# Performance work log

Hardware: AMD Instinct MI355X
Metric: run time of the kernel (lower is better)

The kernel has to match this reference:

```python
import jax, jax.numpy as jnp
import numpy as np

K = 3  # kernel_size
KK = K * K


def conv2d(x, w, b, stride=1, padding=1, dilation=1):
    out = jax.lax.conv_general_dilated(
        x, w, (stride, stride), [(padding, padding), (padding, padding)],
        rhs_dilation=(dilation, dilation),
        dimension_numbers=('NCHW', 'OIHW', 'NCHW'))
    return out + b[None, :, None, None]


def bilinear_gather(x, py, px):
    # x: [B,C,H,W]; py,px: [B,KK,H,W] float sampling coords (zero outside).
    B, C, H, W = x.shape
    y0 = jnp.floor(py)
    x0 = jnp.floor(px)
    wy1 = py - y0
    wx1 = px - x0
    xf = x.reshape(B, C, H * W)

    def corner(yc, xc, wgt):
        valid = (yc >= 0) & (yc <= H - 1) & (xc >= 0) & (xc <= W - 1)
        yi = jnp.clip(yc, 0, H - 1).astype(jnp.int32)
        xi = jnp.clip(xc, 0, W - 1).astype(jnp.int32)
        idx = (yi * W + xi).reshape(B, 1, -1)  # [B,1,KK*H*W]
        v = jnp.take_along_axis(xf, jnp.broadcast_to(idx, (B, C, idx.shape[-1])), axis=2)
        v = v.reshape(B, C, *yc.shape[1:])  # [B,C,KK,H,W]
        return v * (wgt * valid)[:, None]

    return (corner(y0, x0, (1 - wy1) * (1 - wx1)) +
            corner(y0, x0 + 1, (1 - wy1) * wx1) +
            corner(y0 + 1, x0, wy1 * (1 - wx1)) +
            corner(y0 + 1, x0 + 1, wy1 * wx1))


def modulated_deform_conv(x, offset, mask, w, b, stride=1, padding=1, dilation=1):
    B, C, H, W = x.shape
    Ho, Wo = offset.shape[2], offset.shape[3]
    off = offset.reshape(B, KK, 2, Ho, Wo)
    dy, dx = off[:, :, 0], off[:, :, 1]  # [B,KK,Ho,Wo]
    ki, kj = jnp.meshgrid(jnp.arange(K), jnp.arange(K), indexing='ij')
    ki = ki.reshape(-1).astype(x.dtype)  # [KK]
    kj = kj.reshape(-1).astype(x.dtype)
    base_y = (jnp.arange(Ho) * stride - padding).astype(x.dtype)
    base_x = (jnp.arange(Wo) * stride - padding).astype(x.dtype)
    py = base_y[None, None, :, None] + (ki * dilation)[None, :, None, None] + dy
    px = base_x[None, None, None, :] + (kj * dilation)[None, :, None, None] + dx
    x_off = bilinear_gather(x, py, px)              # [B,C,KK,Ho,Wo]
    x_off = x_off * mask[:, None]                   # modulation
    w_flat = w.reshape(w.shape[0], C, KK)           # [O,C,KK]
    out = jnp.einsum('bckhw,ock->bohw', x_off, w_flat)
    return out + b[None, :, None, None]


def setup_inputs() -> dict:
    key = jax.random.key(0)
    ks = jax.random.split(key, 7)
    B, C, O, H, W = 8, 64, 64, 128, 128
    x = jax.random.normal(ks[0], (B, C, H, W), dtype=jnp.float32)
    # offset/mask predictor convs (zero-init in the module; randomized small here
    # so offsets/masks are non-trivial for kernel correctness testing)
    p_w = jax.random.normal(ks[1], (2 * KK, C, 3, 3), dtype=jnp.float32) * 0.02
    p_b = jax.random.normal(ks[2], (2 * KK,), dtype=jnp.float32) * 0.1
    m_w = jax.random.normal(ks[3], (KK, C, 3, 3), dtype=jnp.float32) * 0.02
    m_b = jax.random.normal(ks[4], (KK,), dtype=jnp.float32) * 0.1
    # deformable conv weights
    d_w = jax.random.normal(ks[5], (O, C, K, K), dtype=jnp.float32) * (1.0 / np.sqrt(C * KK))
    d_b = jax.random.normal(ks[6], (O,), dtype=jnp.float32) * 0.01
    return {"x": x, "p_w": p_w, "p_b": p_b, "m_w": m_w, "m_b": m_b, "d_w": d_w, "d_b": d_b}


def reference(x, p_w, p_b, m_w, m_b, d_w, d_b):
    offset = conv2d(x, p_w, p_b, stride=1, padding=1, dilation=1)   # [B,18,H,W]
    mask = jax.nn.sigmoid(conv2d(x, m_w, m_b, stride=1, padding=1, dilation=1))  # [B,9,H,W]
    out = modulated_deform_conv(x, offset, mask, d_w, d_b, stride=1, padding=1, dilation=1)
    return (out, offset)
```

## Files before the change

kernel.cpp:

```cpp
#include <hip/hip_runtime.h>
#include <math.h>

#define KK 9
#define BB 8
#define CC 64
#define OO 64
#define HH 128
#define WW 128
#define HWSZ (HH*WW)

typedef _Float16 half8 __attribute__((ext_vector_type(8)));
typedef float    floatx4 __attribute__((ext_vector_type(4)));

#define WP_ELEMS (32*576)
#define WD_ELEMS (9*64*64)
#define XH_ELEMS ((size_t)BB*HWSZ*64)
#define NCONV 2048

__global__ __launch_bounds__(256) void prep(
    const float* __restrict__ x,
    const float* __restrict__ p_w, const float* __restrict__ m_w,
    const float* __restrict__ d_w,
    _Float16* __restrict__ Wp, _Float16* __restrict__ Wd, _Float16* __restrict__ x_h,
    int conv_blocks)
{
    const int blk = blockIdx.x;
    const int tid = threadIdx.x;
    if (blk < conv_blocks) {
        __shared__ _Float16 sh[64][72];
        const int b    = blk >> 8;
        const int pix0 = (blk & 255) * 64;
        const float* xb = x + (size_t)b*CC*HWSZ + pix0;
        {
            const int p     = tid & 63;
            const int cbase = tid >> 6;
            #pragma unroll
            for (int j = 0; j < 16; ++j) {
                const int c = j*4 + cbase;
                sh[p][c] = (_Float16)xb[(size_t)c*HWSZ + p];
            }
        }
        __syncthreads();
        {
            const int p  = tid >> 2;
            const int c0 = (tid & 3) * 16;
            _Float16* dst = x_h + ((size_t)b*HWSZ + pix0 + p)*64 + c0;
            *(half8*)dst       = *(const half8*)&sh[p][c0];
            *(half8*)(dst + 8) = *(const half8*)&sh[p][c0 + 8];
        }
    } else {
        const int i = (blk - conv_blocks)*256 + tid;
        if (i < WP_ELEMS) {
            int n = i / 576, r = i % 576;
            int k = r >> 6, c = r & 63;
            float v = 0.f;
            if (n < 18)      v = p_w[(n*CC + c)*KK + k];
            else if (n < 27) v = m_w[((n-18)*CC + c)*KK + k];
            Wp[i] = (_Float16)v;
        } else if (i < WP_ELEMS + WD_ELEMS) {
            int j = i - WP_ELEMS;
            int k = j / 4096, r = j % 4096, o = r >> 6, c = r & 63;
            Wd[j] = (_Float16)d_w[(o*CC + c)*KK + k];
        }
    }
}

__global__ __launch_bounds__(512, 4) void dcn_fused(
    const _Float16* __restrict__ x_h,
    const _Float16* __restrict__ Wp, const _Float16* __restrict__ Wd,
    const float* __restrict__ p_b, const float* __restrict__ m_b,
    const float* __restrict__ db,
    float* __restrict__ out, float* __restrict__ offset_out)
{
    __shared__ alignas(16) char smem[128*72*2 + 64*72*2];
    _Float16* AS = (_Float16*)smem;
    _Float16* WS = (_Float16*)(smem + 128*72*2);

    const int tid  = threadIdx.x;
    const int wv   = tid >> 6;
    const int lane = tid & 63;
    const int quad = lane >> 4;
    const int l15  = lane & 15;
    const int p    = tid & 127;
    const int cq   = tid >> 7;
    const int b    = blockIdx.x & 7;
    const int row  = blockIdx.x >> 3;
    const int pix0 = row * WW;
    const _Float16* xbh = x_h + (size_t)b*HWSZ*64;

    half8 q0, q1, pw1;
    bool vldc = false;
    auto issue1 = [&](int k) {
        const int hy = row + k/3 - 1;
        const int wx = p   + k%3 - 1;
        vldc = (hy >= 0) & (hy < HH) & (wx >= 0) & (wx < WW);
        const _Float16* ap = xbh + (size_t)(vldc ? hy*WW + wx : 0)*64 + cq*16;
        q0 = *(const half8*)ap;
        q1 = *(const half8*)(ap + 8);
        if (tid < 256)
            pw1 = *(const half8*)(Wp + (tid>>3)*576 + k*64 + (tid&7)*8);
    };

    floatx4 accp[2];
    accp[0] = (floatx4)0.f; accp[1] = (floatx4)0.f;

    issue1(0);
    #pragma unroll
    for (int k = 0; k < 9; ++k) {
        if (tid < 256)
            *(half8*)&WS[(tid>>3)*72 + (tid&7)*8] = pw1;
        const half8 z = (half8)(_Float16)0.f;
        *(half8*)&AS[p*72 + cq*16]     = vldc ? q0 : z;
        *(half8*)&AS[p*72 + cq*16 + 8] = vldc ? q1 : z;
        __syncthreads();
        if (k < 8) issue1(k+1);
        #pragma unroll
        for (int ks = 0; ks < 2; ++ks) {
            half8 bf0 = *(const half8*)&WS[(l15     )*72 + ks*32 + quad*8];
            half8 bf1 = *(const half8*)&WS[(16 + l15)*72 + ks*32 + quad*8];
            half8 af  = *(const half8*)&AS[(wv*16 + l15)*72 + ks*32 + quad*8];
            accp[0] = __builtin_amdgcn_mfma_f32_16x16x32_f16(af, bf0, accp[0], 0, 0, 0);
            accp[1] = __builtin_amdgcn_mfma_f32_16x16x32_f16(af, bf1, accp[1], 0, 0, 0);
        }
        __syncthreads();
    }

    float* T = (float*)AS;
    #pragma unroll
    for (int nt = 0; nt < 2; ++nt) {
        const int ch = nt*16 + l15;
        if (ch < 27) {
            #pragma unroll
            for (int r = 0; r < 4; ++r)
                T[ch*132 + wv*16 + quad*4 + r] = accp[nt][r];
        }
    }
    __syncthreads();

    float dyk[9], dxk[9], mkk[9];
    #pragma unroll
    for (int k = 0; k < 9; ++k) {
        dyk[k] = T[(2*k  )*132 + p] + p_b[2*k];
        dxk[k] = T[(2*k+1)*132 + p] + p_b[2*k+1];
        mkk[k] = 1.f / (1.f + expf(-(T[(18+k)*132 + p] + m_b[k])));
    }
    {
        float* offp = offset_out + (size_t)b*18*HWSZ + pix0;
        #pragma unroll
        for (int j = 0; j < 5; ++j) {
            const int idx = j*512 + tid;
            if (idx < 2304) {
                const int ch = idx >> 7, px = idx & 127;
                offp[ch*HWSZ + px] = T[ch*132 + px] + p_b[ch];
            }
        }
    }
    __syncthreads();

    half8 pa[8], pwv;
    float phw[4];
    auto issue2 = [&](int k) {
        const float py = (float)(row - 1 + k/3) + dyk[k];
        const float px = (float)(p   - 1 + k%3) + dxk[k];
        const float mk = mkk[k];
        const float y0f = floorf(py), x0f = floorf(px);
        const int   iy0 = (int)y0f,   ix0 = (int)x0f;
        const float wy1 = py - y0f,   wx1 = px - x0f;
        const float wy0 = 1.f - wy1,  wx0 = 1.f - wx1;
        const bool vy0 = (iy0   >= 0) & (iy0   < HH);
        const bool vy1 = (iy0+1 >= 0) & (iy0+1 < HH);
        const bool vx0 = (ix0   >= 0) & (ix0   < WW);
        const bool vx1 = (ix0+1 >= 0) & (ix0+1 < WW);
        const int cy0 = min(max(iy0,   0), HH-1), cy1 = min(max(iy0+1, 0), HH-1);
        const int cx0 = min(max(ix0,   0), WW-1), cx1 = min(max(ix0+1, 0), WW-1);
        const int i0 = cy0*WW+cx0, i1 = cy0*WW+cx1, i2 = cy1*WW+cx0, i3 = cy1*WW+cx1;
        phw[0] = wy0*wx0*((vy0&vx0) ? mk : 0.f);
        phw[1] = wy0*wx1*((vy0&vx1) ? mk : 0.f);
        phw[2] = wy1*wx0*((vy1&vx0) ? mk : 0.f);
        phw[3] = wy1*wx1*((vy1&vx1) ? mk : 0.f);
        const _Float16* c0p = xbh + (size_t)i0*64 + cq*16;
        const _Float16* c1p = xbh + (size_t)i1*64 + cq*16;
        const _Float16* c2p = xbh + (size_t)i2*64 + cq*16;
        const _Float16* c3p = xbh + (size_t)i3*64 + cq*16;
        pa[0] = *(const half8*)c0p;  pa[1] = *(const half8*)(c0p + 8);
        pa[2] = *(const half8*)c1p;  pa[3] = *(const half8*)(c1p + 8);
        pa[4] = *(const half8*)c2p;  pa[5] = *(const half8*)(c2p + 8);
        pa[6] = *(const half8*)c3p;  pa[7] = *(const half8*)(c3p + 8);
        pwv = *(const half8*)(Wd + k*4096 + tid*8);
    };

    floatx4 acc[4];
    #pragma unroll
    for (int nt = 0; nt < 4; ++nt) acc[nt] = (floatx4)0.f;

    issue2(0);
    #pragma unroll
    for (int k = 0; k < 9; ++k) {
        *(half8*)&WS[(tid>>3)*72 + (tid&7)*8] = pwv;
        const _Float16 g0 = (_Float16)phw[0], g1 = (_Float16)phw[1],
                       g2 = (_Float16)phw[2], g3 = (_Float16)phw[3];
        half8 lo = pa[0]*g0 + pa[2]*g1 + pa[4]*g2 + pa[6]*g3;
        half8 hi = pa[1]*g0 + pa[3]*g1 + pa[5]*g2 + pa[7]*g3;
        *(half8*)&AS[p*72 + cq*16]     = lo;
        *(half8*)&AS[p*72 + cq*16 + 8] = hi;
        __syncthreads();
        if (k < 8) issue2(k+1);
        #pragma unroll
        for (int ks = 0; ks < 2; ++ks) {
            half8 af = *(const half8*)&AS[(wv*16 + l15)*72 + ks*32 + quad*8];
            #pragma unroll
            for (int nt = 0; nt < 4; ++nt) {
                half8 bf = *(const half8*)&WS[(nt*16 + l15)*72 + ks*32 + quad*8];
                acc[nt] = __builtin_amdgcn_mfma_f32_16x16x32_f16(af, bf, acc[nt], 0, 0, 0);
            }
        }
        __syncthreads();
    }

    float* T2 = (float*)AS;
    #pragma unroll
    for (int oc = 0; oc < 4; ++oc) {
        #pragma unroll
        for (int r = 0; r < 4; ++r)
            T2[l15*132 + wv*16 + quad*4 + r] = acc[oc][r];
        __syncthreads();
        #pragma unroll
        for (int j = 0; j < 4; ++j) {
            const int idx = j*512 + tid;
            const int o16 = idx >> 7, p2 = idx & 127;
            out[((size_t)b*OO + oc*16 + o16)*HWSZ + pix0 + p2] = T2[o16*132 + p2] + db[oc*16 + o16];
        }
        __syncthreads();
    }
}

__global__ __launch_bounds__(256, 4) void dcn_fused_lds(
    const float* __restrict__ x,
    const _Float16* __restrict__ Wp, const _Float16* __restrict__ Wd,
    const float* __restrict__ p_b, const float* __restrict__ m_b,
    const float* __restrict__ db,
    float* __restrict__ out, float* __restrict__ offset_out)
{
    __shared__ alignas(16) _Float16 A_sh[128][72];
    __shared__ alignas(16) _Float16 WM_sh[32*72];
    __shared__ alignas(16) _Float16 Wd_sh[64][72];

    const int tid   = threadIdx.x;
    const int wv    = tid >> 6;
    const int lane  = tid & 63;
    const int quad  = lane >> 4;
    const int l15   = lane & 15;
    const int b     = blockIdx.x & 7;
    const int row   = blockIdx.x >> 3;
    const int pix0  = row * WW;
    const int p     = tid & 127;
    const int chalf = (tid >> 7) * 32;
    const int h = row, w = p;
    const float* xb = x + (size_t)b*CC*HWSZ;
    _Float16 (*W_sh)[72] = (_Float16 (*)[72])WM_sh;

    floatx4 accp[2][2];
    #pragma unroll
    for (int mt = 0; mt < 2; ++mt)
        #pragma unroll
        for (int nt = 0; nt < 2; ++nt) accp[mt][nt] = (floatx4)0.f;

    for (int k = 0; k < 9; ++k) {
        {
            const int n  = tid >> 3;
            const int c0 = (tid & 7) * 8;
            *(half8*)&W_sh[n][c0] = *(const half8*)(Wp + n*576 + k*64 + c0);
        }
        const int hy = h + (k/3) - 1;
        const int wx = w + (k%3) - 1;
        const bool vld = (hy >= 0) & (hy < HH) & (wx >= 0) & (wx < WW);
        const float* xs = xb + hy*WW + wx;
        #pragma unroll
        for (int cb = 0; cb < 4; ++cb) {
            union { half8 v; _Float16 e[8]; } u;
            #pragma unroll
            for (int j = 0; j < 8; ++j)
                u.e[j] = (_Float16)(vld ? xs[(size_t)(chalf + cb*8 + j)*HWSZ] : 0.f);
            *(half8*)&A_sh[p][chalf + cb*8] = u.v;
        }
        __syncthreads();
        #pragma unroll
        for (int ks = 0; ks < 2; ++ks) {
            half8 bf[2];
            #pragma unroll
            for (int nt = 0; nt < 2; ++nt)
                bf[nt] = *(const half8*)&W_sh[nt*16 + l15][ks*32 + quad*8];
            #pragma unroll
            for (int mt = 0; mt < 2; ++mt) {
                half8 af = *(const half8*)&A_sh[wv*32 + mt*16 + l15][ks*32 + quad*8];
                accp[mt][0] = __builtin_amdgcn_mfma_f32_16x16x32_f16(af, bf[0], accp[mt][0], 0, 0, 0);
                accp[mt][1] = __builtin_amdgcn_mfma_f32_16x16x32_f16(af, bf[1], accp[mt][1], 0, 0, 0);
            }
        }
        __syncthreads();
    }

    float (*T)[132] = (float (*)[132])&A_sh[0][0];
    #pragma unroll
    for (int nt = 0; nt < 2; ++nt) {
        const int ch = nt*16 + l15;
        if (ch < 27) {
            #pragma unroll
            for (int mt = 0; mt < 2; ++mt)
                #pragma unroll
                for (int r = 0; r < 4; ++r)
                    T[ch][wv*32 + mt*16 + quad*4 + r] = accp[mt][nt][r];
        }
    }
    __syncthreads();

    float dyk[9], dxk[9], mkk[9];
    float* offp = offset_out + (size_t)b*18*HWSZ + pix0;
    #pragma unroll
    for (int k = 0; k < 9; ++k) {
        dyk[k] = T[2*k][p]   + p_b[2*k];
        dxk[k] = T[2*k+1][p] + p_b[2*k+1];
        mkk[k] = 1.f / (1.f + expf(-(T[18+k][p] + m_b[k])));
    }
    if (tid < 128) {
        #pragma unroll
        for (int k = 0; k < 9; ++k) {
            offp[(2*k  )*HWSZ + p] = dyk[k];
            offp[(2*k+1)*HWSZ + p] = dxk[k];
        }
    }
    __syncthreads();

    floatx4 acc[2][4];
    #pragma unroll
    for (int mt = 0; mt < 2; ++mt)
        #pragma unroll
        for (int nt = 0; nt < 4; ++nt) acc[mt][nt] = (floatx4)0.f;

    for (int k = 0; k < 9; ++k) {
        {
            const int o  = tid >> 2;
            const int c0 = (tid & 3) * 16;
            const _Float16* src = Wd + k*4096 + o*64 + c0;
            *(half8*)&Wd_sh[o][c0]     = *(const half8*)src;
            *(half8*)&Wd_sh[o][c0 + 8] = *(const half8*)(src + 8);
        }
        const float mk = mkk[k];
        const float py = (float)(h - 1 + k/3) + dyk[k];
        const float px = (float)(w - 1 + k%3) + dxk[k];
        const float y0f = floorf(py), x0f = floorf(px);
        const int   iy0 = (int)y0f,   ix0 = (int)x0f;
        const float wy1 = py - y0f,   wx1 = px - x0f;
        const float wy0 = 1.f - wy1,  wx0 = 1.f - wx1;
        const bool vy0 = (iy0   >= 0) & (iy0   < HH);
        const bool vy1 = (iy0+1 >= 0) & (iy0+1 < HH);
        const bool vx0 = (ix0   >= 0) & (ix0   < WW);
        const bool vx1 = (ix0+1 >= 0) & (ix0+1 < WW);
        const int cy0 = min(max(iy0,   0), HH-1), cy1 = min(max(iy0+1, 0), HH-1);
        const int cx0 = min(max(ix0,   0), WW-1), cx1 = min(max(ix0+1, 0), WW-1);
        const int i0 = cy0*WW+cx0; const float w0 = wy0*wx0*((vy0&vx0) ? mk : 0.f);
        const int i1 = cy0*WW+cx1; const float w1 = wy0*wx1*((vy0&vx1) ? mk : 0.f);
        const int i2 = cy1*WW+cx0; const float w2 = wy1*wx0*((vy1&vx0) ? mk : 0.f);
        const int i3 = cy1*WW+cx1; const float w3 = wy1*wx1*((vy1&vx1) ? mk : 0.f);
        #pragma unroll
        for (int cb = 0; cb < 4; ++cb) {
            union { half8 v; _Float16 e[8]; } u;
            #pragma unroll
            for (int j = 0; j < 8; ++j) {
                const float* xc = xb + (size_t)(chalf + cb*8 + j)*HWSZ;
                u.e[j] = (_Float16)(w0*xc[i0] + w1*xc[i1] + w2*xc[i2] + w3*xc[i3]);
            }
            *(half8*)&A_sh[p][chalf + cb*8] = u.v;
        }
        __syncthreads();
        #pragma unroll
        for (int ks = 0; ks < 2; ++ks) {
            half8 bf[4];
            #pragma unroll
            for (int nt = 0; nt < 4; ++nt)
                bf[nt] = *(const half8*)&Wd_sh[nt*16 + l15][ks*32 + quad*8];
            #pragma unroll
            for (int mt = 0; mt < 2; ++mt) {
                half8 af = *(const half8*)&A_sh[wv*32 + mt*16 + l15][ks*32 + quad*8];
                #pragma unroll
                for (int nt = 0; nt < 4; ++nt)
                    acc[mt][nt] = __builtin_amdgcn_mfma_f32_16x16x32_f16(af, bf[nt], acc[mt][nt], 0, 0, 0);
            }
        }
        __syncthreads();
    }

    float (*T2)[132] = (float (*)[132])&A_sh[0][0];
    #pragma unroll
    for (int oc = 0; oc < 4; ++oc) {
        #pragma unroll
        for (int mt = 0; mt < 2; ++mt)
            #pragma unroll
            for (int r = 0; r < 4; ++r)
                T2[l15][wv*32 + mt*16 + quad*4 + r] = acc[mt][oc][r];
        __syncthreads();
        #pragma unroll
        for (int j = 0; j < 8; ++j) {
            const int idx = tid + j*256;
            const int o16 = idx >> 7, p2 = idx & 127;
            out[((size_t)b*OO + oc*16 + o16)*HWSZ + pix0 + p2] = T2[o16][p2] + db[oc*16 + o16];
        }
        __syncthreads();
    }
}

extern "C" void kernel_launch(void* const* d_in, const int* in_sizes, int n_in,
                              void* d_out, int out_size, void* d_ws, size_t ws_size,
                              hipStream_t stream) {
    const float* x   = (const float*)d_in[0];
    const float* p_w = (const float*)d_in[1];
    const float* p_b = (const float*)d_in[2];
    const float* m_w = (const float*)d_in[3];
    const float* m_b = (const float*)d_in[4];
    const float* dw  = (const float*)d_in[5];
    const float* db  = (const float*)d_in[6];

    float* out        = (float*)d_out;
    float* offset_out = out + (size_t)BB*OO*HWSZ;

    _Float16* Wp  = (_Float16*)d_ws;
    _Float16* Wd  = Wp + WP_ELEMS;
    _Float16* x_h = Wd + WD_ELEMS;

    const int nrep = (WP_ELEMS + WD_ELEMS + 255) / 256;
    const size_t need = (size_t)(WP_ELEMS + WD_ELEMS + XH_ELEMS) * sizeof(_Float16);
    if (ws_size >= need) {
        prep<<<dim3(NCONV + nrep), 256, 0, stream>>>(x, p_w, m_w, dw, Wp, Wd, x_h, NCONV);
        dcn_fused<<<dim3(128*BB), 512, 0, stream>>>(x_h, Wp, Wd, p_b, m_b, db, out, offset_out);
    } else {
        prep<<<dim3(nrep), 256, 0, stream>>>(x, p_w, m_w, dw, Wp, Wd, x_h, 0);
        dcn_fused_lds<<<dim3(128*BB), 256, 0, stream>>>(x, Wp, Wd, p_b, m_b, db, out, offset_out);
    }
}
```

Before: 184.1 us.

## Pre-swizzle weights into MFMA fragment order and load operands directly from global

The prep kernel now writes the predictor and deform weights in the per-lane MFMA fragment layout, so the fused kernel reads A and B operands straight from global memory instead of staging them through LDS. The fused kernel is retiled to half-row blocks of 64 pixels with 256 threads, twice as many blocks, and only the deform weights are double-buffered in LDS with one barrier per tap. Offset and mask values are read from a shared table per tap instead of held in registers, and the bias is folded in once. This removes most LDS traffic and barriers, in exchange for more redundant global gathers of x_h per pixel tile and more blocks that each reload the weights.

Measured after the change: 187.9 us. +2.1%, slower.

```diff
diff --git a/kernel.cpp b/kernel.cpp
--- a/kernel.cpp
+++ b/kernel.cpp
@@ -12,8 +12,8 @@
 typedef _Float16 half8 __attribute__((ext_vector_type(8)));
 typedef float    floatx4 __attribute__((ext_vector_type(4)));
 
-#define WP_ELEMS (32*576)
-#define WD_ELEMS (9*64*64)
+#define WP_ELEMS (9*2*4*32*8)
+#define WD_ELEMS (9*2*4*64*8)
 #define XH_ELEMS ((size_t)BB*HWSZ*64)
 #define NCONV 2048
 
@@ -51,184 +51,173 @@
     } else {
         const int i = (blk - conv_blocks)*256 + tid;
         if (i < WP_ELEMS) {
-            int n = i / 576, r = i % 576;
-            int k = r >> 6, c = r & 63;
+            const int e = i & 7, n = (i>>3)&31, quad = (i>>8)&3, ks = (i>>10)&1, k = i>>11;
+            const int c = ks*32 + quad*8 + e;
             float v = 0.f;
             if (n < 18)      v = p_w[(n*CC + c)*KK + k];
             else if (n < 27) v = m_w[((n-18)*CC + c)*KK + k];
             Wp[i] = (_Float16)v;
         } else if (i < WP_ELEMS + WD_ELEMS) {
-            int j = i - WP_ELEMS;
-            int k = j / 4096, r = j % 4096, o = r >> 6, c = r & 63;
+            const int j = i - WP_ELEMS;
+            const int e = j & 7, o = (j>>3)&63, quad = (j>>9)&3, ks = (j>>11)&1, k = j>>12;
+            const int c = ks*32 + quad*8 + e;
             Wd[j] = (_Float16)d_w[(o*CC + c)*KK + k];
         }
     }
 }
 
-__global__ __launch_bounds__(512, 4) void dcn_fused(
+__global__ __launch_bounds__(256, 4) void dcn_fused(
     const _Float16* __restrict__ x_h,
     const _Float16* __restrict__ Wp, const _Float16* __restrict__ Wd,
     const float* __restrict__ p_b, const float* __restrict__ m_b,
     const float* __restrict__ db,
     float* __restrict__ out, float* __restrict__ offset_out)
 {
-    __shared__ alignas(16) char smem[128*72*2 + 64*72*2];
-    _Float16* AS = (_Float16*)smem;
-    _Float16* WS = (_Float16*)(smem + 128*72*2);
+    __shared__ alignas(16) float    T[27*68];
+    __shared__ alignas(16) _Float16 WS[2][4096];
 
     const int tid  = threadIdx.x;
     const int wv   = tid >> 6;
     const int lane = tid & 63;
     const int quad = lane >> 4;
     const int l15  = lane & 15;
-    const int p    = tid & 127;
-    const int cq   = tid >> 7;
     const int b    = blockIdx.x & 7;
-    const int row  = blockIdx.x >> 3;
-    const int pix0 = row * WW;
+    const int seg  = blockIdx.x >> 3;
+    const int row  = seg >> 1;
+    const int col0 = (seg & 1) * 64;
+    const int pix0 = row * WW + col0;
+    const int px   = wv*16 + l15;
+    const int wx   = col0 + px;
     const _Float16* xbh = x_h + (size_t)b*HWSZ*64;
 
-    half8 q0, q1, pw1;
-    bool vldc = false;
-    auto issue1 = [&](int k) {
-        const int hy = row + k/3 - 1;
-        const int wx = p   + k%3 - 1;
-        vldc = (hy >= 0) & (hy < HH) & (wx >= 0) & (wx < WW);
-        const _Float16* ap = xbh + (size_t)(vldc ? hy*WW + wx : 0)*64 + cq*16;
-        q0 = *(const half8*)ap;
-        q1 = *(const half8*)(ap + 8);
-        if (tid < 256)
-            pw1 = *(const half8*)(Wp + (tid>>3)*576 + k*64 + (tid&7)*8);
-    };
+    half8 ws0a = *(const half8*)(Wd + tid*16);
+    half8 ws0b = *(const half8*)(Wd + tid*16 + 8);
 
     floatx4 accp[2];
     accp[0] = (floatx4)0.f; accp[1] = (floatx4)0.f;
-
-    issue1(0);
     #pragma unroll
     for (int k = 0; k < 9; ++k) {
-        if (tid < 256)
-            *(half8*)&WS[(tid>>3)*72 + (tid&7)*8] = pw1;
+        const int hy = row + k/3 - 1;
+        const int hx = wx  + k%3 - 1;
+        const bool vld = (hy >= 0) & (hy < HH) & (hx >= 0) & (hx < WW);
+        const _Float16* ap = xbh + (size_t)(vld ? hy*WW + hx : 0)*64 + quad*8;
         const half8 z = (half8)(_Float16)0.f;
-        *(half8*)&AS[p*72 + cq*16]     = vldc ? q0 : z;
-        *(half8*)&AS[p*72 + cq*16 + 8] = vldc ? q1 : z;
-        __syncthreads();
-        if (k < 8) issue1(k+1);
+        half8 a0 = *(const half8*)ap;
+        half8 a1 = *(const half8*)(ap + 32);
+        a0 = vld ? a0 : z;
+        a1 = vld ? a1 : z;
+        const _Float16* wp = Wp + k*2048 + quad*256 + l15*8;
         #pragma unroll
         for (int ks = 0; ks < 2; ++ks) {
-            half8 bf0 = *(const half8*)&WS[(l15     )*72 + ks*32 + quad*8];
-            half8 bf1 = *(const half8*)&WS[(16 + l15)*72 + ks*32 + quad*8];
-            half8 af  = *(const half8*)&AS[(wv*16 + l15)*72 + ks*32 + quad*8];
-            accp[0] = __builtin_amdgcn_mfma_f32_16x16x32_f16(af, bf0, accp[0], 0, 0, 0);
-            accp[1] = __builtin_amdgcn_mfma_f32_16x16x32_f16(af, bf1, accp[1], 0, 0, 0);
-        }
-        __syncthreads();
-    }
-
-    float* T = (float*)AS;
+            const half8 af = ks ? a1 : a0;
+            accp[0] = __builtin_amdgcn_mfma_f32_16x16x32_f16(af, *(const half8*)(wp + ks*1024),       accp[0], 0, 0, 0);
+            accp[1] = __builtin_amdgcn_mfma_f32_16x16x32_f16(af, *(const half8*)(wp + ks*1024 + 128), accp[1], 0, 0, 0);
+        }
+    }
+
     #pragma unroll
     for (int nt = 0; nt < 2; ++nt) {
         const int ch = nt*16 + l15;
         if (ch < 27) {
+            const float bias = (ch < 18) ? p_b[ch] : m_b[ch-18];
             #pragma unroll
             for (int r = 0; r < 4; ++r)
-                T[ch*132 + wv*16 + quad*4 + r] = accp[nt][r];
-        }
+                T[ch*68 + wv*16 + quad*4 + r] = accp[nt][r] + bias;
+        }
+    }
+    {
+        _Float16* wd = &WS[0][tid*16];
+        *(half8*)wd     = ws0a;
+        *(half8*)(wd+8) = ws0b;
     }
     __syncthreads();
 
-    float dyk[9], dxk[9], mkk[9];
-    #pragma unroll
-    for (int k = 0; k < 9; ++k) {
-        dyk[k] = T[(2*k  )*132 + p] + p_b[2*k];
-        dxk[k] = T[(2*k+1)*132 + p] + p_b[2*k+1];
-        mkk[k] = 1.f / (1.f + expf(-(T[(18+k)*132 + p] + m_b[k])));
-    }
     {
         float* offp = offset_out + (size_t)b*18*HWSZ + pix0;
         #pragma unroll
         for (int j = 0; j < 5; ++j) {
-            const int idx = j*512 + tid;
-            if (idx < 2304) {
-                const int ch = idx >> 7, px = idx & 127;
-                offp[ch*HWSZ + px] = T[ch*132 + px] + p_b[ch];
+            const int idx = j*256 + tid;
+            if (idx < 18*64) {
+                const int ch = idx >> 6, p2 = idx & 63;
+                offp[ch*HWSZ + p2] = T[ch*68 + p2];
             }
         }
     }
-    __syncthreads();
-
-    half8 pa[8], pwv;
-    float phw[4];
-    auto issue2 = [&](int k) {
-        const float py = (float)(row - 1 + k/3) + dyk[k];
-        const float px = (float)(p   - 1 + k%3) + dxk[k];
-        const float mk = mkk[k];
-        const float y0f = floorf(py), x0f = floorf(px);
+
+    floatx4 acc[4];
+    #pragma unroll
+    for (int nt = 0; nt < 4; ++nt) acc[nt] = (floatx4)0.f;
+
+    #pragma unroll
+    for (int k = 0; k < 9; ++k) {
+        half8 wsa, wsb;
+        if (k < 8) {
+            const _Float16* wsrc = Wd + (k+1)*4096 + tid*16;
+            wsa = *(const half8*)wsrc;
+            wsb = *(const half8*)(wsrc + 8);
+        }
+
+        const float dy = T[(2*k  )*68 + px];
+        const float dx = T[(2*k+1)*68 + px];
+        const float mk = 1.f / (1.f + expf(-T[(18+k)*68 + px]));
+        const float py  = (float)(row - 1 + k/3) + dy;
+        const float pxf = (float)(wx  - 1 + k%3) + dx;
+        const float y0f = floorf(py), x0f = floorf(pxf);
         const int   iy0 = (int)y0f,   ix0 = (int)x0f;
-        const float wy1 = py - y0f,   wx1 = px - x0f;
+        const float wy1 = py - y0f,   wx1 = pxf - x0f;
         const float wy0 = 1.f - wy1,  wx0 = 1.f - wx1;
-        const bool vy0 = (iy0   >= 0) & (iy0   < HH);
-        const bool vy1 = (iy0+1 >= 0) & (iy0+1 < HH);
-        const bool vx0 = (ix0   >= 0) & (ix0   < WW);
-        const bool vx1 = (ix0+1 >= 0) & (ix0+1 < WW);
+        const bool vy0 = ((unsigned)iy0     < (unsigned)HH);
+        const bool vy1 = ((unsigned)(iy0+1) < (unsigned)HH);
+        const bool vx0 = ((unsigned)ix0     < (unsigned)WW);
+        const bool vx1 = ((unsigned)(ix0+1) < (unsigned)WW);
         const int cy0 = min(max(iy0,   0), HH-1), cy1 = min(max(iy0+1, 0), HH-1);
         const int cx0 = min(max(ix0,   0), WW-1), cx1 = min(max(ix0+1, 0), WW-1);
         const int i0 = cy0*WW+cx0, i1 = cy0*WW+cx1, i2 = cy1*WW+cx0, i3 = cy1*WW+cx1;
-        phw[0] = wy0*wx0*((vy0&vx0) ? mk : 0.f);
-        phw[1] = wy0*wx1*((vy0&vx1) ? mk : 0.f);
-        phw[2] = wy1*wx0*((vy1&vx0) ? mk : 0.f);
-        phw[3] = wy1*wx1*((vy1&vx1) ? mk : 0.f);
-        const _Float16* c0p = xbh + (size_t)i0*64 + cq*16;
-        const _Float16* c1p = xbh + (size_t)i1*64 + cq*16;
-        const _Float16* c2p = xbh + (size_t)i2*64 + cq*16;
-        const _Float16* c3p = xbh + (size_t)i3*64 + cq*16;
-        pa[0] = *(const half8*)c0p;  pa[1] = *(const half8*)(c0p + 8);
-        pa[2] = *(const half8*)c1p;  pa[3] = *(const half8*)(c1p + 8);
-        pa[4] = *(const half8*)c2p;  pa[5] = *(const half8*)(c2p + 8);
-        pa[6] = *(const half8*)c3p;  pa[7] = *(const half8*)(c3p + 8);
-        pwv = *(const half8*)(Wd + k*4096 + tid*8);
-    };
-
-    floatx4 acc[4];
-    #pragma unroll
-    for (int nt = 0; nt < 4; ++nt) acc[nt] = (floatx4)0.f;
-
-    issue2(0);
-    #pragma unroll
-    for (int k = 0; k < 9; ++k) {
-        *(half8*)&WS[(tid>>3)*72 + (tid&7)*8] = pwv;
-        const _Float16 g0 = (_Float16)phw[0], g1 = (_Float16)phw[1],
-                       g2 = (_Float16)phw[2], g3 = (_Float16)phw[3];
-        half8 lo = pa[0]*g0 + pa[2]*g1 + pa[4]*g2 + pa[6]*g3;
-        half8 hi = pa[1]*g0 + pa[3]*g1 + pa[5]*g2 + pa[7]*g3;
-        *(half8*)&AS[p*72 + cq*16]     = lo;
-        *(half8*)&AS[p*72 + cq*16 + 8] = hi;
-        __syncthreads();
-        if (k < 8) issue2(k+1);
+        const _Float16 g0 = (_Float16)(wy0*wx0*((vy0&vx0) ? mk : 0.f));
+        const _Float16 g1 = (_Float16)(wy0*wx1*((vy0&vx1) ? mk : 0.f));
+        const _Float16 g2 = (_Float16)(wy1*wx0*((vy1&vx0) ? mk : 0.f));
+        const _Float16 g3 = (_Float16)(wy1*wx1*((vy1&vx1) ? mk : 0.f));
+
+        const _Float16* c0p = xbh + (size_t)i0*64 + quad*8;
+        const _Float16* c1p = xbh + (size_t)i1*64 + quad*8;
+        const _Float16* c2p = xbh + (size_t)i2*64 + quad*8;
+        const _Float16* c3p = xbh + (size_t)i3*64 + quad*8;
+        const half8 p0l = *(const half8*)c0p, p0h = *(const half8*)(c0p + 32);
+        const half8 p1l = *(const half8*)c1p, p1h = *(const half8*)(c1p + 32);
+        const half8 p2l = *(const half8*)c2p, p2h = *(const half8*)(c2p + 32);
+        const half8 p3l = *(const half8*)c3p, p3h = *(const half8*)(c3p + 32);
+        const half8 lo = p0l*g0 + p1l*g1 + p2l*g2 + p3l*g3;
+        const half8 hi = p0h*g0 + p1h*g1 + p2h*g2 + p3h*g3;
+
         #pragma unroll
         for (int ks = 0; ks < 2; ++ks) {
-            half8 af = *(const half8*)&AS[(wv*16 + l15)*72 + ks*32 + quad*8];
-            #pragma unroll
-            for (int nt = 0; nt < 4; ++nt) {
-                half8 bf = *(const half8*)&WS[(nt*16 + l15)*72 + ks*32 + quad*8];
-                acc[nt] = __builtin_amdgcn_mfma_f32_16x16x32_f16(af, bf, acc[nt], 0, 0, 0);
-            }
-        }
-        __syncthreads();
-    }
-
-    float* T2 = (float*)AS;
+            const half8 af = ks ? hi : lo;
+            const _Float16* wsp = &WS[k&1][ks*2048 + quad*512 + l15*8];
+            #pragma unroll
+            for (int nt = 0; nt < 4; ++nt)
+                acc[nt] = __builtin_amdgcn_mfma_f32_16x16x32_f16(af, *(const half8*)(wsp + nt*128), acc[nt], 0, 0, 0);
+        }
+
+        if (k < 8) {
+            _Float16* wd = &WS[(k+1)&1][tid*16];
+            *(half8*)wd     = wsa;
+            *(half8*)(wd+8) = wsb;
+        }
+        __syncthreads();
+    }
+
+    float* T2 = (float*)&WS[0][0];
     #pragma unroll
     for (int oc = 0; oc < 4; ++oc) {
         #pragma unroll
         for (int r = 0; r < 4; ++r)
-            T2[l15*132 + wv*16 + quad*4 + r] = acc[oc][r];
+            T2[l15*68 + wv*16 + quad*4 + r] = acc[oc][r];
         __syncthreads();
         #pragma unroll
         for (int j = 0; j < 4; ++j) {
-            const int idx = j*512 + tid;
-            const int o16 = idx >> 7, p2 = idx & 127;
-            out[((size_t)b*OO + oc*16 + o16)*HWSZ + pix0 + p2] = T2[o16*132 + p2] + db[oc*16 + o16];
+            const int idx = j*256 + tid;
+            const int o16 = idx >> 6, p2 = idx & 63;
+            out[((size_t)b*OO + oc*16 + o16)*HWSZ + pix0 + p2] = T2[o16*68 + p2] + db[oc*16 + o16];
         }
         __syncthreads();
     }
@@ -269,7 +258,8 @@
         {
             const int n  = tid >> 3;
             const int c0 = (tid & 7) * 8;
-            *(half8*)&W_sh[n][c0] = *(const half8*)(Wp + n*576 + k*64 + c0);
+            *(half8*)&W_sh[n][c0] =
+                *(const half8*)(Wp + k*2048 + (c0>>5)*1024 + ((c0>>3)&3)*256 + n*8);
         }
         const int hy = h + (k/3) - 1;
         const int wx = w + (k%3) - 1;
@@ -341,9 +331,11 @@
         {
             const int o  = tid >> 2;
             const int c0 = (tid & 3) * 16;
-            const _Float16* src = Wd + k*4096 + o*64 + c0;
-            *(half8*)&Wd_sh[o][c0]     = *(const half8*)src;
-            *(half8*)&Wd_sh[o][c0 + 8] = *(const half8*)(src + 8);
+            *(half8*)&Wd_sh[o][c0] =
+                *(const half8*)(Wd + k*4096 + (c0>>5)*2048 + ((c0>>3)&3)*512 + o*8);
+            const int c8 = c0 + 8;
+            *(half8*)&Wd_sh[o][c8] =
+                *(const half8*)(Wd + k*4096 + (c8>>5)*2048 + ((c8>>3)&3)*512 + o*8);
         }
         const float mk = mkk[k];
         const float py = (float)(h - 1 + k/3) + dyk[k];
@@ -431,7 +423,7 @@
     const size_t need = (size_t)(WP_ELEMS + WD_ELEMS + XH_ELEMS) * sizeof(_Float16);
     if (ws_size >= need) {
         prep<<<dim3(NCONV + nrep), 256, 0, stream>>>(x, p_w, m_w, dw, Wp, Wd, x_h, NCONV);
-        dcn_fused<<<dim3(128*BB), 512, 0, stream>>>(x_h, Wp, Wd, p_b, m_b, db, out, offset_out);
+        dcn_fused<<<dim3(256*BB), 256, 0, stream>>>(x_h, Wp, Wd, p_b, m_b, db, out, offset_out);
     } else {
         prep<<<dim3(nrep), 256, 0, stream>>>(x, p_w, m_w, dw, Wp, Wd, x_h, 0);
         dcn_fused_lds<<<dim3(128*BB), 256, 0, stream>>>(x, Wp, Wd, p_b, m_b, db, out, offset_out);
```
